# Kernel optimization log

Hardware: AMD Instinct MI355X
Metric: run time of the kernel (lower is better)

## Reference

```python
import jax, jax.numpy as jnp
import numpy as np
import itertools

KH = KW = 3
N_NZ = 5
K_OUT = 126  # C(9,5) -> all patterns, matches capped n_kernels
C_IN = 128


def setup_inputs() -> dict:
    key = jax.random.key(0)
    k1, k2 = jax.random.split(key)
    inputs = jax.random.normal(k1, (32, 112, 112, C_IN), dtype=jnp.float32)
    # sparse_kernel: (n_non_zero, in_channels, kernels), glorot-ish scale
    scale = (2.0 / (N_NZ * C_IN + K_OUT)) ** 0.5
    sparse_kernel = jax.random.normal(k2, (N_NZ, C_IN, K_OUT), dtype=jnp.float32) * scale
    bias = jnp.zeros((K_OUT,), dtype=jnp.float32)
    # deterministic unique sparsity patterns: all C(9,5) flat-position combos
    patterns = jnp.asarray(
        np.array(list(itertools.combinations(range(KH * KW), N_NZ)), dtype=np.int32)
    )  # (K_OUT, N_NZ) flat positions in [0, 9)
    return {"inputs": inputs, "sparse_kernel": sparse_kernel, "bias": bias, "patterns": patterns}


def reference(inputs, sparse_kernel, bias, patterns):
    k_out = patterns.shape[0]
    c_in = sparse_kernel.shape[1]
    kk = jnp.arange(k_out)[:, None]  # (K,1) broadcasts against (K,N)
    # scatter: dense_flat[pos, :, k] = sparse_kernel[n, :, k]
    updates = jnp.transpose(sparse_kernel, (2, 0, 1))  # (K, N, Cin)
    dense_flat = jnp.zeros((KH * KW, c_in, k_out), dtype=inputs.dtype)
    dense_flat = dense_flat.at[patterns, :, kk].set(updates)
    dense_kernel = dense_flat.reshape(KH, KW, c_in, k_out)
    out = jax.lax.conv_general_dilated(
        inputs, dense_kernel, window_strides=(1, 1), padding="SAME",
        dimension_numbers=("NHWC", "HWIO", "NHWC"))
    return jax.nn.relu(out + bias)
```

## Files before the change

### kernel.cpp

```cpp
#include <hip/hip_runtime.h>


typedef __attribute__((ext_vector_type(8))) __bf16 bf16x8;
typedef __attribute__((ext_vector_type(4))) float f32x4;
typedef __attribute__((ext_vector_type(8))) unsigned short ushort8;

__device__ __forceinline__ unsigned short f2bf(float f) {
  unsigned int u = __builtin_bit_cast(unsigned int, f);
  u += 0x7fffu + ((u >> 16) & 1u);
  return (unsigned short)(u >> 16);
}

__device__ __forceinline__ unsigned int cvt_pk_bf16(float lo, float hi) {
  unsigned int r;
  asm("v_cvt_pk_bf16_f32 %0, %1, %2" : "=v"(r) : "v"(lo), "v"(hi));
  return r;
}

__device__ __forceinline__ void async_copy16(void* lds, const void* g) {
  __builtin_amdgcn_global_load_lds(
      (const __attribute__((address_space(1))) unsigned int*)g,
      (__attribute__((address_space(3))) unsigned int*)lds, 16, 0, 0);
}

#define BWS_BYTES 294912
#define ROW_BYTES 29184
#define ROW_USH   14592
#define AIN_BYTES (3584LL * ROW_BYTES)
#define WS_NEED   ((size_t)BWS_BYTES + (size_t)AIN_BYTES + (size_t)ROW_BYTES)

__global__ __launch_bounds__(256) void build_B(const float* __restrict__ sk,
                                               const int* __restrict__ patterns,
                                               unsigned short* __restrict__ Bws) {
  int idx = blockIdx.x * 256 + threadIdx.x;
  if (idx >= 9 * 128 * 128) return;
  int c = idx & 127;
  int n = (idx >> 7) & 127;
  int p = idx >> 14;
  float v = 0.f;
  if (n < 126) {
#pragma unroll
    for (int j = 0; j < 5; ++j)
      if (patterns[n * 5 + j] == p) v = sk[(j * 128 + c) * 126 + n];
  }
  int cc = c >> 5, cl = c & 31;
  Bws[(((p * 4 + cc) * 128) + n) * 32 + cl] = f2bf(v);
}

__global__ __launch_bounds__(256) void conv_pre(const float* __restrict__ in,
                                                unsigned short* __restrict__ Ain) {
  __shared__ unsigned short T[112 * 136];
  const int bid = ((blockIdx.x & 7) * 448) + (blockIdx.x >> 3);
  const float* inrow = in + (size_t)bid * 112 * 128;
  unsigned short* orow = Ain + (size_t)bid * ROW_USH;
  const int tid = threadIdx.x;
#pragma unroll
  for (int it = 0; it < 14; ++it) {
    int i = tid + it * 256;
    int px = i >> 5, c4 = i & 31;
    float4 v = *(const float4*)(inrow + (size_t)i * 4);
    unsigned int lo = cvt_pk_bf16(v.x, v.y);
    unsigned int hi = cvt_pk_bf16(v.z, v.w);
    *(uint2*)&T[px * 136 + c4 * 4] = make_uint2(lo, hi);
  }
  __syncthreads();
#pragma unroll
  for (int it = 0; it < 8; ++it) {
    int o = tid + it * 256;
    if (o < 1824) {
      int ccq = o / 114;
      int px = o - ccq * 114;
      int gx = px - 1;
      ushort8 s = (ushort8)0;
      if ((unsigned)gx < 112u) s = *(const ushort8*)&T[gx * 136 + ccq * 8];
      *(ushort8*)(orow + (size_t)o * 8) = s;
    }
  }
}

__global__ __launch_bounds__(256, 2) void conv_main(const unsigned short* __restrict__ Ain,
                                                    const unsigned short* __restrict__ zp,
                                                    const unsigned short* __restrict__ Bws,
                                                    const float* __restrict__ bias,
                                                    float* __restrict__ out) {
  __shared__ unsigned short Alds[2 * 1536 * 8];

  const int tid = threadIdx.x;
  const int bid = ((blockIdx.x & 7) * 448) + (blockIdx.x >> 3);
  const int y = bid % 112;
  const int lane = tid & 63;
  const int w = tid >> 6;
  const int wm = w >> 1;
  const int wn = w & 1;
  const int quad = lane >> 4;
  const int lrow = lane & 15;

  const unsigned short* rp1 = Ain + (size_t)bid * ROW_USH;
  const unsigned short* rp0 = (y > 0)   ? (rp1 - ROW_USH) : zp;
  const unsigned short* rp2 = (y < 111) ? (rp1 + ROW_USH) : zp;

  f32x4 acc[4][4];
#pragma unroll
  for (int mt = 0; mt < 4; ++mt)
#pragma unroll
    for (int j = 0; j < 4; ++j) acc[mt][j] = (f32x4)0.f;

  auto stage = [&](int cc, int buf) {
    const unsigned short* c0 = rp0 + cc * 3648;
    const unsigned short* c1 = rp1 + cc * 3648;
    const unsigned short* c2 = rp2 + cc * 3648;
#pragma unroll
    for (int it = 0; it < 6; ++it) {
      int i = tid + it * 256;
      bool b1 = (i >= 456), b2 = (i >= 912);
      int rem = i - (b2 ? 912 : (b1 ? 456 : 0));
      const unsigned short* base = b2 ? c2 : (b1 ? c1 : c0);
      const unsigned short* src = (i < 1368) ? (base + rem * 8) : zp;
      async_copy16((void*)&Alds[(size_t)buf * 12288 + (size_t)i * 8], (const void*)src);
    }
  };

  stage(0, 0);
  __syncthreads();

#pragma unroll 1
  for (int cc = 0; cc < 4; ++cc) {
    const int buf = cc & 1;
    bf16x8 b[9][4];
    const unsigned short* Bb = Bws + (size_t)cc * 4096 + (wn * 64 + lrow) * 32 + quad * 8;
#pragma unroll
    for (int p = 0; p < 9; ++p)
#pragma unroll
      for (int j = 0; j < 4; ++j)
        b[p][j] = *(const bf16x8*)(Bb + p * 16384 + j * 512);

    if (cc < 3) stage(cc + 1, buf ^ 1);

#pragma unroll
    for (int p = 0; p < 9; ++p) {
      const int r = p / 3;
      const int dx = p - r * 3;
      const int abase = buf * 12288 + r * 3648 + quad * 912 + (dx + lrow) * 8 + wm * 512;
#pragma unroll
      for (int mt = 0; mt < 4; ++mt) {
        if (mt < 3 || wm == 0) {
          bf16x8 a = *(const bf16x8*)&Alds[abase + mt * 128];
#pragma unroll
          for (int j = 0; j < 4; ++j)
            acc[mt][j] = __builtin_amdgcn_mfma_f32_16x16x32_bf16(a, b[p][j], acc[mt][j], 0, 0, 0);
        }
      }
    }

    if (cc < 3) __syncthreads();
  }

  const int kb = wn * 64 + lrow;
  float bv[4];
#pragma unroll
  for (int j = 0; j < 4; ++j) {
    int k = kb + j * 16;
    bv[j] = bias[k < 126 ? k : 125];
  }
  float* outrow = out + (size_t)bid * 112 * 126;
#pragma unroll
  for (int mt = 0; mt < 4; ++mt) {
    if (mt < 3 || wm == 0) {
#pragma unroll
      for (int rg = 0; rg < 4; ++rg) {
        int x = wm * 64 + mt * 16 + quad * 4 + rg;
        float* o = outrow + (size_t)x * 126;
#pragma unroll
        for (int j = 0; j < 4; ++j) {
          int k = kb + j * 16;
          if (k < 126) { float v = acc[mt][j][rg] + bv[j]; o[k] = v > 0.f ? v : 0.f; }
        }
      }
    }
  }
}

__global__ __launch_bounds__(256, 2) void conv_main_fb(const float* __restrict__ in,
                                                       const unsigned short* __restrict__ Bws,
                                                       const float* __restrict__ bias,
                                                       float* __restrict__ out) {
  __shared__ unsigned short Alds[2 * 4 * 342 * 8];

  const int tid = threadIdx.x;
  const int bid = ((blockIdx.x & 7) * 448) + (blockIdx.x >> 3);
  const int nimg = bid / 112;
  const int y = bid - nimg * 112;
  const int lane = tid & 63;
  const int w = tid >> 6;
  const int quad = lane >> 4;
  const int lrow = lane & 15;

  const float* inb = in + (size_t)nimg * 112 * 112 * 128;

  f32x4 acc[7][2];
#pragma unroll
  for (int mt = 0; mt < 7; ++mt) { acc[mt][0] = (f32x4)0.f; acc[mt][1] = (f32x4)0.f; }

  float4 pf[11];
  auto loadA = [&](int cc) {
#pragma unroll
    for (int it = 0; it < 11; ++it) {
      int i = tid + it * 256;
      float4 v = make_float4(0.f, 0.f, 0.f, 0.f);
      if (i < 2736) {
        int c4 = i & 7;
        int rest = i >> 3;
        int r = rest / 114;
        int hx = rest - r * 114;
        int gy = y + r - 1;
        int gx = hx - 1;
        if ((unsigned)gy < 112u && (unsigned)gx < 112u)
          v = *(const float4*)(inb + ((size_t)gy * 112 + gx) * 128 + cc * 32 + c4 * 4);
      }
      pf[it] = v;
    }
  };
  auto writeA = [&](int b) {
#pragma unroll
    for (int it = 0; it < 11; ++it) {
      int i = tid + it * 256;
      if (i < 2736) {
        int c4 = i & 7;
        int rest = i >> 3;
        int q = c4 >> 1, h = c4 & 1;
        ushort4 s;
        s.x = f2bf(pf[it].x); s.y = f2bf(pf[it].y);
        s.z = f2bf(pf[it].z); s.w = f2bf(pf[it].w);
        *(ushort4*)&Alds[(((b * 4 + q) * 342) + rest) * 8 + h * 4] = s;
      }
    }
  };

  loadA(0);
  writeA(0);
  __syncthreads();

#pragma unroll 1
  for (int cc = 0; cc < 4; ++cc) {
    const int cur = cc & 1;
    bf16x8 b[9][2];
#pragma unroll
    for (int p = 0; p < 9; ++p)
#pragma unroll
      for (int j = 0; j < 2; ++j)
        b[p][j] = *(const bf16x8*)(Bws +
            (((size_t)(p * 4 + cc) * 128 + w * 32 + j * 16 + lrow) * 32 + quad * 8));

    if (cc < 3) loadA(cc + 1);

    const unsigned short* Ab = &Alds[(size_t)(cur * 4 + quad) * 2736];
#pragma unroll
    for (int p = 0; p < 9; ++p) {
      const int r = p / 3;
      const int px = p - r * 3;
      const int abase = (r * 114 + px + lrow) * 8;
#pragma unroll
      for (int mt = 0; mt < 7; ++mt) {
        bf16x8 a = *(const bf16x8*)&Ab[abase + mt * 128];
        acc[mt][0] = __builtin_amdgcn_mfma_f32_16x16x32_bf16(a, b[p][0], acc[mt][0], 0, 0, 0);
        acc[mt][1] = __builtin_amdgcn_mfma_f32_16x16x32_bf16(a, b[p][1], acc[mt][1], 0, 0, 0);
      }
    }

    if (cc < 3) {
      writeA(cur ^ 1);
      __syncthreads();
    }
  }

  const int k0 = w * 32 + lrow;
  const int k1 = k0 + 16;
  const float bv0 = bias[k0 < 126 ? k0 : 125];
  const float bv1 = bias[k1 < 126 ? k1 : 125];
  float* outrow = out + (size_t)bid * 112 * 126;
#pragma unroll
  for (int mt = 0; mt < 7; ++mt) {
#pragma unroll
    for (int rg = 0; rg < 4; ++rg) {
      int x = mt * 16 + quad * 4 + rg;
      float* o = outrow + (size_t)x * 126;
      if (k0 < 126) { float v = acc[mt][0][rg] + bv0; o[k0] = v > 0.f ? v : 0.f; }
      if (k1 < 126) { float v = acc[mt][1][rg] + bv1; o[k1] = v > 0.f ? v : 0.f; }
    }
  }
}

extern "C" void kernel_launch(void* const* d_in, const int* in_sizes, int n_in,
                              void* d_out, int out_size, void* d_ws, size_t ws_size,
                              hipStream_t stream) {
  const float* in = (const float*)d_in[0];
  const float* sk = (const float*)d_in[1];
  const float* bias = (const float*)d_in[2];
  const int* patterns = (const int*)d_in[3];
  float* out = (float*)d_out;
  unsigned short* Bws = (unsigned short*)d_ws;

  build_B<<<dim3(576), dim3(256), 0, stream>>>(sk, patterns, Bws);

  if (ws_size >= WS_NEED) {
    unsigned short* Ain = (unsigned short*)((char*)d_ws + BWS_BYTES);
    unsigned short* zp  = (unsigned short*)((char*)d_ws + BWS_BYTES + AIN_BYTES);
    hipMemsetAsync(zp, 0, ROW_BYTES, stream);
    conv_pre<<<dim3(32 * 112), dim3(256), 0, stream>>>(in, Ain);
    conv_main<<<dim3(32 * 112), dim3(256), 0, stream>>>(Ain, zp, Bws, bias, out);
  } else {
    conv_main_fb<<<dim3(32 * 112), dim3(256), 0, stream>>>(in, Bws, bias, out);
  }
}
```

Baseline: 507.6 us.

## Store padded input pixel-major and gather channel chunks during LDS staging

```diff
diff --git a/kernel.cpp b/kernel.cpp
--- a/kernel.cpp
+++ b/kernel.cpp
@@ -49,31 +49,27 @@
 
 __global__ __launch_bounds__(256) void conv_pre(const float* __restrict__ in,
                                                 unsigned short* __restrict__ Ain) {
-  __shared__ unsigned short T[112 * 136];
   const int bid = ((blockIdx.x & 7) * 448) + (blockIdx.x >> 3);
   const float* inrow = in + (size_t)bid * 112 * 128;
   unsigned short* orow = Ain + (size_t)bid * ROW_USH;
   const int tid = threadIdx.x;
 #pragma unroll
-  for (int it = 0; it < 14; ++it) {
+  for (int it = 0; it < 8; ++it) {
     int i = tid + it * 256;
-    int px = i >> 5, c4 = i & 31;
-    float4 v = *(const float4*)(inrow + (size_t)i * 4);
-    unsigned int lo = cvt_pk_bf16(v.x, v.y);
-    unsigned int hi = cvt_pk_bf16(v.z, v.w);
-    *(uint2*)&T[px * 136 + c4 * 4] = make_uint2(lo, hi);
-  }
-  __syncthreads();
-#pragma unroll
-  for (int it = 0; it < 8; ++it) {
-    int o = tid + it * 256;
-    if (o < 1824) {
-      int ccq = o / 114;
-      int px = o - ccq * 114;
+    if (i < 1824) {
+      int px = i >> 4, c8 = i & 15;
       int gx = px - 1;
-      ushort8 s = (ushort8)0;
-      if ((unsigned)gx < 112u) s = *(const ushort8*)&T[gx * 136 + ccq * 8];
-      *(ushort8*)(orow + (size_t)o * 8) = s;
+      uint4 u = make_uint4(0u, 0u, 0u, 0u);
+      if ((unsigned)gx < 112u) {
+        const float* p = inrow + ((size_t)gx * 128) + c8 * 8;
+        float4 a = *(const float4*)p;
+        float4 b = *(const float4*)(p + 4);
+        u.x = cvt_pk_bf16(a.x, a.y);
+        u.y = cvt_pk_bf16(a.z, a.w);
+        u.z = cvt_pk_bf16(b.x, b.y);
+        u.w = cvt_pk_bf16(b.z, b.w);
+      }
+      *(uint4*)(orow + (size_t)i * 8) = u;
     }
   }
 }
@@ -83,7 +79,7 @@
                                                     const unsigned short* __restrict__ Bws,
                                                     const float* __restrict__ bias,
                                                     float* __restrict__ out) {
-  __shared__ unsigned short Alds[2 * 1536 * 8];
+  __shared__ unsigned short Alds[2 * 11040 + 64];
 
   const int tid = threadIdx.x;
   const int bid = ((blockIdx.x & 7) * 448) + (blockIdx.x >> 3);
@@ -96,8 +92,23 @@
   const int lrow = lane & 15;
 
   const unsigned short* rp1 = Ain + (size_t)bid * ROW_USH;
-  const unsigned short* rp0 = (y > 0)   ? (rp1 - ROW_USH) : zp;
-  const unsigned short* rp2 = (y < 111) ? (rp1 + ROW_USH) : zp;
+  const int zpOff = (int)(3584 - bid) * ROW_USH;
+  const int r0Off = (y > 0)   ? -ROW_USH : zpOff;
+  const int r2Off = (y < 111) ?  ROW_USH : zpOff;
+
+  int soff[6];
+#pragma unroll
+  for (int it = 0; it < 6; ++it) {
+    int i = tid + it * 256;
+    int t = i / 115;
+    int px = i - t * 115;
+    int q = t & 3;
+    int r = t >> 2;
+    int off;
+    if (px >= 114 || t >= 12) off = zpOff;
+    else off = (r == 0 ? r0Off : (r == 1 ? 0 : r2Off)) + px * 128 + q * 8;
+    soff[it] = off;
+  }
 
   f32x4 acc[4][4];
 #pragma unroll
@@ -106,17 +117,12 @@
     for (int j = 0; j < 4; ++j) acc[mt][j] = (f32x4)0.f;
 
   auto stage = [&](int cc, int buf) {
-    const unsigned short* c0 = rp0 + cc * 3648;
-    const unsigned short* c1 = rp1 + cc * 3648;
-    const unsigned short* c2 = rp2 + cc * 3648;
+    unsigned short* dst = &Alds[buf * 11040 + tid * 8];
+    const unsigned short* s = rp1 + cc * 32;
 #pragma unroll
     for (int it = 0; it < 6; ++it) {
-      int i = tid + it * 256;
-      bool b1 = (i >= 456), b2 = (i >= 912);
-      int rem = i - (b2 ? 912 : (b1 ? 456 : 0));
-      const unsigned short* base = b2 ? c2 : (b1 ? c1 : c0);
-      const unsigned short* src = (i < 1368) ? (base + rem * 8) : zp;
-      async_copy16((void*)&Alds[(size_t)buf * 12288 + (size_t)i * 8], (const void*)src);
+      if (it < 5 || tid < 100)
+        async_copy16((void*)(dst + it * 2048), (const void*)(s + soff[it]));
     }
   };
 
@@ -133,14 +139,16 @@
 #pragma unroll
       for (int j = 0; j < 4; ++j)
         b[p][j] = *(const bf16x8*)(Bb + p * 16384 + j * 512);
+    asm volatile("s_waitcnt vmcnt(0)" ::: "memory");
 
     if (cc < 3) stage(cc + 1, buf ^ 1);
 
+    const int abase0 = buf * 11040 + quad * 920 + (wm * 64 + lrow) * 8;
 #pragma unroll
     for (int p = 0; p < 9; ++p) {
       const int r = p / 3;
       const int dx = p - r * 3;
-      const int abase = buf * 12288 + r * 3648 + quad * 912 + (dx + lrow) * 8 + wm * 512;
+      const int abase = abase0 + r * 3680 + dx * 8;
 #pragma unroll
       for (int mt = 0; mt < 4; ++mt) {
         if (mt < 3 || wm == 0) {
@@ -184,7 +192,7 @@
                                                        const unsigned short* __restrict__ Bws,
                                                        const float* __restrict__ bias,
                                                        float* __restrict__ out) {
-  __shared__ unsigned short Alds[2 * 4 * 342 * 8];
+  __shared__ unsigned short AldsF[2 * 4 * 342 * 8];
 
   const int tid = threadIdx.x;
   const int bid = ((blockIdx.x & 7) * 448) + (blockIdx.x >> 3);
@@ -231,7 +239,7 @@
         ushort4 s;
         s.x = f2bf(pf[it].x); s.y = f2bf(pf[it].y);
         s.z = f2bf(pf[it].z); s.w = f2bf(pf[it].w);
-        *(ushort4*)&Alds[(((b * 4 + q) * 342) + rest) * 8 + h * 4] = s;
+        *(ushort4*)&AldsF[(((b * 4 + q) * 342) + rest) * 8 + h * 4] = s;
       }
     }
   };
@@ -253,7 +261,7 @@
 
     if (cc < 3) loadA(cc + 1);
 
-    const unsigned short* Ab = &Alds[(size_t)(cur * 4 + quad) * 2736];
+    const unsigned short* Ab = &AldsF[(size_t)(cur * 4 + quad) * 2736];
 #pragma unroll
     for (int p = 0; p < 9; ++p) {
       const int r = p / 3;
```

After: 538.5 us. 6.1% more time.
